# Kernel tuning notes

Measured on AMD Instinct MI355X. Metric: run time of the kernel, lower is better.

## Reference

```python
import jax, jax.numpy as jnp
import numpy as np

M, IN, OUT, R = 8192, 4096, 4096, 16  # tokens, in_features, out_features, lora rank


def setup_inputs() -> dict:
    key = jax.random.key(0)
    k = jax.random.split(key, 7)
    # symmetric int8 quantized activations and weights
    x = jax.random.randint(k[0], (M, IN), -127, 128, dtype=jnp.int8)
    weight = jax.random.randint(k[1], (OUT, IN), -127, 128, dtype=jnp.int8)
    # per-token activation scales and per-output-channel weight scales
    x_scales = jax.random.uniform(k[2], (M,), jnp.float32, 0.5, 1.5) / 127.0
    scales = jax.random.uniform(k[3], (OUT,), jnp.float32, 0.5, 1.5) / 127.0
    bias = jax.random.normal(k[4], (OUT,), jnp.float32)
    # module inits lora_a ~ N(0, 1/r); lora_b is zeros in the module but we use
    # small random values so the LoRA path is numerically exercised
    lora_a = jax.random.normal(k[5], (R, IN), jnp.float32) * (1.0 / R)
    lora_b = jax.random.normal(k[6], (OUT, R), jnp.float32) * 0.02
    return dict(x=x, weight=weight, bias=bias, x_scales=x_scales,
                scales=scales, lora_a=lora_a, lora_b=lora_b, fuse_gelu=1)


def reference(x, weight, bias, x_scales, scales, lora_a, lora_b, fuse_gelu):
    acc = jax.lax.dot_general(x, weight, (((1,), (1,)), ((), ())),
                              preferred_element_type=jnp.int32)
    # dequantize with outer product of per-token and per-channel scales
    main = acc.astype(jnp.float32) * x_scales[:, None] * scales[None, :]
    # LoRA correction on the dequantized activations: (x_deq @ A^T) @ B^T
    x_deq = x.astype(jnp.float32) * x_scales[:, None]          # [M, IN]
    lora = (x_deq @ lora_a.T) @ lora_b.T                        # [M, R] @ [R, OUT]
    out = main + lora + bias[None, :]
    if fuse_gelu:  # static Python flag
        out = jax.nn.gelu(out, approximate=True)  # tanh-approx GELU (CUDA fused path)
    return out
```

## Files before the change

kernel.cpp:

```cpp
#include <hip/hip_runtime.h>

#define M_DIM 8192
#define IN_DIM 4096
#define OUT_DIM 4096

typedef int   v4i __attribute__((ext_vector_type(4)));
typedef short v8s __attribute__((ext_vector_type(8)));
typedef float v4f __attribute__((ext_vector_type(4)));

static __device__ __forceinline__ int pack4(int a, int b, int c, int d) {
    return (a & 255) | ((b & 255) << 8) | ((c & 255) << 16) | ((d & 255) << 24);
}

static __device__ __forceinline__ short f2bf(float f) {
    unsigned u = __float_as_uint(f);
    u = (u + 0x7FFFu + ((u >> 16) & 1u)) >> 16;
    return (short)u;
}

static __device__ __forceinline__ float gelu_tanh(float u) {
    float u2 = u * u;
    float p  = fmaf(u2, 0.0356774081f, 0.7978845608f);
    float v  = u * p;
    float e  = __builtin_amdgcn_exp2f(v * 2.8853900818f);
    float d  = e + 1.0f;
    return u - u * __builtin_amdgcn_rcpf(d);
}

static __device__ __forceinline__ void async_cp16(const signed char* g, signed char* l) {
    __builtin_amdgcn_global_load_lds((const __attribute__((address_space(1))) void*)g,
                                     (__attribute__((address_space(3))) void*)l, 16, 0, 0);
}

__global__ __launch_bounds__(256) void pack_w_kernel(const int* __restrict__ w,
                                                     signed char* __restrict__ w8) {
    size_t i = ((size_t)blockIdx.x * 256 + threadIdx.x) * 16;
    const int4* p = (const int4*)(w + i);
    int4 a = p[0], b = p[1], c = p[2], d = p[3];
    int4 o;
    o.x = pack4(a.x, a.y, a.z, a.w);
    o.y = pack4(b.x, b.y, b.z, b.w);
    o.z = pack4(c.x, c.y, c.z, c.w);
    o.w = pack4(d.x, d.y, d.z, d.w);
    *(int4*)(w8 + i) = o;
}

__global__ __launch_bounds__(256) void pack_x_lora_kernel(const int* __restrict__ x,
                                                          const float* __restrict__ la,
                                                          signed char* __restrict__ x8,
                                                          float* __restrict__ T) {
    __shared__ float red[64 * 257];
    const int t    = threadIdx.x;
    const int row0 = blockIdx.x * 4;
    const int k0   = t * 16;

    float xf[4][16];
#pragma unroll
    for (int g = 0; g < 4; ++g) {
        const int4* xp = (const int4*)(x + (size_t)(row0 + g) * IN_DIM + k0);
        int4 a = xp[0], b = xp[1], c = xp[2], d = xp[3];
        int4 o;
        o.x = pack4(a.x, a.y, a.z, a.w);
        o.y = pack4(b.x, b.y, b.z, b.w);
        o.z = pack4(c.x, c.y, c.z, c.w);
        o.w = pack4(d.x, d.y, d.z, d.w);
        *(int4*)(x8 + (size_t)(row0 + g) * IN_DIM + k0) = o;
        xf[g][0]=(float)a.x;  xf[g][1]=(float)a.y;  xf[g][2]=(float)a.z;  xf[g][3]=(float)a.w;
        xf[g][4]=(float)b.x;  xf[g][5]=(float)b.y;  xf[g][6]=(float)b.z;  xf[g][7]=(float)b.w;
        xf[g][8]=(float)c.x;  xf[g][9]=(float)c.y;  xf[g][10]=(float)c.z; xf[g][11]=(float)c.w;
        xf[g][12]=(float)d.x; xf[g][13]=(float)d.y; xf[g][14]=(float)d.z; xf[g][15]=(float)d.w;
    }

    float acc[4][16];
#pragma unroll
    for (int g = 0; g < 4; ++g)
#pragma unroll
        for (int r = 0; r < 16; ++r) acc[g][r] = 0.0f;

#pragma unroll
    for (int r = 0; r < 16; ++r) {
        const float4* ap = (const float4*)(la + (size_t)r * IN_DIM + k0);
        float4 a0 = ap[0], a1 = ap[1], a2 = ap[2], a3 = ap[3];
        float av[16] = {a0.x,a0.y,a0.z,a0.w, a1.x,a1.y,a1.z,a1.w,
                        a2.x,a2.y,a2.z,a2.w, a3.x,a3.y,a3.z,a3.w};
#pragma unroll
        for (int g = 0; g < 4; ++g) {
#pragma unroll
            for (int j = 0; j < 16; ++j) acc[g][r] = fmaf(xf[g][j], av[j], acc[g][r]);
        }
    }

#pragma unroll
    for (int g = 0; g < 4; ++g)
#pragma unroll
        for (int r = 0; r < 16; ++r) red[(g * 16 + r) * 257 + t] = acc[g][r];
    __syncthreads();

    if (t < 64) {
        float s = 0.0f;
        for (int tt = 0; tt < 256; ++tt) s += red[t * 257 + tt];
        T[(size_t)(row0 + (t >> 4)) * 16 + (t & 15)] = s;
    }
}

__global__ __launch_bounds__(256) void q8_gemm_kernel(
    const signed char* __restrict__ x8, const signed char* __restrict__ w8,
    const float* __restrict__ T, const float* __restrict__ lb,
    const float* __restrict__ bias, const float* __restrict__ xsc,
    const float* __restrict__ wsc, const int* __restrict__ gflag,
    float* __restrict__ out) {
    __shared__ __align__(16) signed char Ald[128 * 64];
    __shared__ __align__(16) signed char Bld[128 * 64];
    __shared__ __align__(16) short Tb[128 * 32];
    __shared__ __align__(16) short Bb[128 * 32];
    __shared__ float xs_t[128], ws_t[128], bias_t[128];

    const int tid  = threadIdx.x;
    const int lane = tid & 63;
    const int wv   = tid >> 6;
    const int wm   = wv >> 1;
    const int wn   = wv & 1;
    const int bn   = blockIdx.x & 31;
    const int bm   = blockIdx.x >> 5;

    const int frow = lane & 15;
    const int fq   = lane >> 4;

    const int srow = wv * 32 + (lane >> 2);
    const int scol = (lane & 3) * 16;
    const signed char* ag0 = x8 + (size_t)(bm * 128 + srow) * IN_DIM + scol;
    const signed char* ag1 = ag0 + 16 * IN_DIM;
    const signed char* bg0 = w8 + (size_t)(bn * 128 + srow) * IN_DIM + scol;
    const signed char* bg1 = bg0 + 16 * IN_DIM;
    signed char* al0 = &Ald[wv * 2048];
    signed char* al1 = al0 + 1024;
    signed char* bl0 = &Bld[wv * 2048];
    signed char* bl1 = bl0 + 1024;

    v4i acc[4][4];
#pragma unroll
    for (int i = 0; i < 4; ++i)
#pragma unroll
        for (int j = 0; j < 4; ++j) acc[i][j] = 0;

    const int abase = (wm * 64 + frow) * 64 + fq * 16;
    const int bbase = (wn * 64 + frow) * 64 + fq * 16;

    for (int kk = 0; kk < IN_DIM / 64; ++kk) {
        __syncthreads();
        const size_t ko = (size_t)kk * 64;
        async_cp16(ag0 + ko, al0);
        async_cp16(ag1 + ko, al1);
        async_cp16(bg0 + ko, bl0);
        async_cp16(bg1 + ko, bl1);
        __syncthreads();

        v4i av[4], bv[4];
#pragma unroll
        for (int mt = 0; mt < 4; ++mt) av[mt] = *(const v4i*)(Ald + abase + mt * 1024);
#pragma unroll
        for (int nt = 0; nt < 4; ++nt) bv[nt] = *(const v4i*)(Bld + bbase + nt * 1024);
#pragma unroll
        for (int mt = 0; mt < 4; ++mt)
#pragma unroll
            for (int nt = 0; nt < 4; ++nt)
                acc[mt][nt] = __builtin_amdgcn_mfma_i32_16x16x64_i8(av[mt], bv[nt],
                                                                    acc[mt][nt], 0, 0, 0);
    }

    {
        const int row = tid >> 1, half = tid & 1;
        const float4* tp = (const float4*)(T + (size_t)(bm * 128 + row) * 16 + half * 8);
        float4 f0 = tp[0], f1 = tp[1];
        short* dst = &Tb[row * 32 + half * 8];
        dst[0] = f2bf(f0.x); dst[1] = f2bf(f0.y); dst[2] = f2bf(f0.z); dst[3] = f2bf(f0.w);
        dst[4] = f2bf(f1.x); dst[5] = f2bf(f1.y); dst[6] = f2bf(f1.z); dst[7] = f2bf(f1.w);
        short* dz = &Tb[row * 32 + 16 + half * 8];
#pragma unroll
        for (int j = 0; j < 8; ++j) dz[j] = 0;

        const float4* bp = (const float4*)(lb + (size_t)(bn * 128 + row) * 16 + half * 8);
        float4 g0 = bp[0], g1 = bp[1];
        short* db = &Bb[row * 32 + half * 8];
        db[0] = f2bf(g0.x); db[1] = f2bf(g0.y); db[2] = f2bf(g0.z); db[3] = f2bf(g0.w);
        db[4] = f2bf(g1.x); db[5] = f2bf(g1.y); db[6] = f2bf(g1.z); db[7] = f2bf(g1.w);
        short* dbz = &Bb[row * 32 + 16 + half * 8];
#pragma unroll
        for (int j = 0; j < 8; ++j) dbz[j] = 0;
    }
    if (tid < 128) {
        xs_t[tid]   = xsc[bm * 128 + tid];
        ws_t[tid]   = wsc[bn * 128 + tid];
        bias_t[tid] = bias[bn * 128 + tid];
    }
    __syncthreads();

    const bool dg = (*gflag) != 0;

    v8s tb[4], bbf[4];
#pragma unroll
    for (int mt = 0; mt < 4; ++mt)
        tb[mt] = *(const v8s*)(&Tb[(wm * 64 + mt * 16 + frow) * 32 + fq * 8]);
#pragma unroll
    for (int nt = 0; nt < 4; ++nt)
        bbf[nt] = *(const v8s*)(&Bb[(wn * 64 + nt * 16 + frow) * 32 + fq * 8]);

#pragma unroll
    for (int mt = 0; mt < 4; ++mt) {
#pragma unroll
        for (int nt = 0; nt < 4; ++nt) {
            const int ncol  = wn * 64 + nt * 16 + frow;
            const float wsv = ws_t[ncol];
            const float bv  = bias_t[ncol];
            v4f fa;
            fa[0] = (float)acc[mt][nt][0] * wsv;
            fa[1] = (float)acc[mt][nt][1] * wsv;
            fa[2] = (float)acc[mt][nt][2] * wsv;
            fa[3] = (float)acc[mt][nt][3] * wsv;
            fa = __builtin_amdgcn_mfma_f32_16x16x32_bf16(tb[mt], bbf[nt], fa, 0, 0, 0);
#pragma unroll
            for (int r = 0; r < 4; ++r) {
                const int ml = wm * 64 + mt * 16 + fq * 4 + r;
                float u = fmaf(xs_t[ml], fa[r], bv);
                if (dg) u = gelu_tanh(u);
                out[(size_t)(bm * 128 + ml) * OUT_DIM + bn * 128 + ncol] = u;
            }
        }
    }
}

extern "C" void kernel_launch(void* const* d_in, const int* in_sizes, int n_in,
                              void* d_out, int out_size, void* d_ws, size_t ws_size,
                              hipStream_t stream) {
    const int*   x     = (const int*)d_in[0];
    const int*   wt    = (const int*)d_in[1];
    const float* bias  = (const float*)d_in[2];
    const float* xsc   = (const float*)d_in[3];
    const float* wsc   = (const float*)d_in[4];
    const float* la    = (const float*)d_in[5];
    const float* lb    = (const float*)d_in[6];
    const int*   gflag = (const int*)d_in[7];
    float* out = (float*)d_out;

    signed char* x8 = (signed char*)d_ws;
    signed char* w8 = x8 + (size_t)M_DIM * IN_DIM;
    float* T = (float*)(w8 + (size_t)OUT_DIM * IN_DIM);

    pack_w_kernel<<<(OUT_DIM * (size_t)IN_DIM) / (16 * 256), 256, 0, stream>>>(wt, w8);
    pack_x_lora_kernel<<<M_DIM / 4, 256, 0, stream>>>(x, la, x8, T);
    q8_gemm_kernel<<<(M_DIM / 128) * (OUT_DIM / 128), 256, 0, stream>>>(
        x8, w8, T, lb, bias, xsc, wsc, gflag, out);
}
```

Measured before the change: 482.7 us.

## Double-buffer GEMM LDS tiles, swizzle layout, and move LoRA projection to MFMA

The int8 GEMM main loop now double-buffers its A/B tiles in a single shared buffer and issues the next k-tile's async loads before computing on the current one. An XOR swizzle on the column offset is meant to cut LDS bank conflicts, and an occupancy hint is added to launch bounds. The LoRA down-projection moves out of a scalar FMA kernel with a large shared reduction into a bf16 MFMA kernel over packed int8 x, with lora_a pre-converted to bf16 in the w8 scratch region before w is packed. The pack kernels are rewritten for coalesced access. Converting x and lora_a to bf16 in the LoRA path changes precision.

```diff
diff --git a/kernel.cpp b/kernel.cpp
--- a/kernel.cpp
+++ b/kernel.cpp
@@ -16,6 +16,11 @@
     unsigned u = __float_as_uint(f);
     u = (u + 0x7FFFu + ((u >> 16) & 1u)) >> 16;
     return (short)u;
+}
+
+static __device__ __forceinline__ short i2bf(int v) {
+    float f = (float)v;
+    return (short)(__float_as_uint(f) >> 16);
 }
 
 static __device__ __forceinline__ float gelu_tanh(float u) {
@@ -23,8 +28,7 @@
     float p  = fmaf(u2, 0.0356774081f, 0.7978845608f);
     float v  = u * p;
     float e  = __builtin_amdgcn_exp2f(v * 2.8853900818f);
-    float d  = e + 1.0f;
-    return u - u * __builtin_amdgcn_rcpf(d);
+    return u - u * __builtin_amdgcn_rcpf(e + 1.0f);
 }
 
 static __device__ __forceinline__ void async_cp16(const signed char* g, signed char* l) {
@@ -32,88 +36,71 @@
                                      (__attribute__((address_space(3))) void*)l, 16, 0, 0);
 }
 
-__global__ __launch_bounds__(256) void pack_w_kernel(const int* __restrict__ w,
-                                                     signed char* __restrict__ w8) {
-    size_t i = ((size_t)blockIdx.x * 256 + threadIdx.x) * 16;
-    const int4* p = (const int4*)(w + i);
-    int4 a = p[0], b = p[1], c = p[2], d = p[3];
-    int4 o;
-    o.x = pack4(a.x, a.y, a.z, a.w);
-    o.y = pack4(b.x, b.y, b.z, b.w);
-    o.z = pack4(c.x, c.y, c.z, c.w);
-    o.w = pack4(d.x, d.y, d.z, d.w);
-    *(int4*)(w8 + i) = o;
-}
-
-__global__ __launch_bounds__(256) void pack_x_lora_kernel(const int* __restrict__ x,
-                                                          const float* __restrict__ la,
-                                                          signed char* __restrict__ x8,
-                                                          float* __restrict__ T) {
-    __shared__ float red[64 * 257];
-    const int t    = threadIdx.x;
-    const int row0 = blockIdx.x * 4;
-    const int k0   = t * 16;
-
-    float xf[4][16];
-#pragma unroll
-    for (int g = 0; g < 4; ++g) {
-        const int4* xp = (const int4*)(x + (size_t)(row0 + g) * IN_DIM + k0);
-        int4 a = xp[0], b = xp[1], c = xp[2], d = xp[3];
-        int4 o;
-        o.x = pack4(a.x, a.y, a.z, a.w);
-        o.y = pack4(b.x, b.y, b.z, b.w);
-        o.z = pack4(c.x, c.y, c.z, c.w);
-        o.w = pack4(d.x, d.y, d.z, d.w);
-        *(int4*)(x8 + (size_t)(row0 + g) * IN_DIM + k0) = o;
-        xf[g][0]=(float)a.x;  xf[g][1]=(float)a.y;  xf[g][2]=(float)a.z;  xf[g][3]=(float)a.w;
-        xf[g][4]=(float)b.x;  xf[g][5]=(float)b.y;  xf[g][6]=(float)b.z;  xf[g][7]=(float)b.w;
-        xf[g][8]=(float)c.x;  xf[g][9]=(float)c.y;  xf[g][10]=(float)c.z; xf[g][11]=(float)c.w;
-        xf[g][12]=(float)d.x; xf[g][13]=(float)d.y; xf[g][14]=(float)d.z; xf[g][15]=(float)d.w;
-    }
-
-    float acc[4][16];
-#pragma unroll
-    for (int g = 0; g < 4; ++g)
-#pragma unroll
-        for (int r = 0; r < 16; ++r) acc[g][r] = 0.0f;
-
-#pragma unroll
-    for (int r = 0; r < 16; ++r) {
-        const float4* ap = (const float4*)(la + (size_t)r * IN_DIM + k0);
-        float4 a0 = ap[0], a1 = ap[1], a2 = ap[2], a3 = ap[3];
-        float av[16] = {a0.x,a0.y,a0.z,a0.w, a1.x,a1.y,a1.z,a1.w,
-                        a2.x,a2.y,a2.z,a2.w, a3.x,a3.y,a3.z,a3.w};
-#pragma unroll
-        for (int g = 0; g < 4; ++g) {
-#pragma unroll
-            for (int j = 0; j < 16; ++j) acc[g][r] = fmaf(xf[g][j], av[j], acc[g][r]);
-        }
-    }
-
-#pragma unroll
-    for (int g = 0; g < 4; ++g)
-#pragma unroll
-        for (int r = 0; r < 16; ++r) red[(g * 16 + r) * 257 + t] = acc[g][r];
+__global__ __launch_bounds__(256) void pack_i32_i8_kernel(const int* __restrict__ src,
+                                                          signed char* __restrict__ dst) {
+    const int t = threadIdx.x;
+    const size_t blk = (size_t)blockIdx.x;
+    const int4* p = (const int4*)src + blk * 1024;
+    int* q = (int*)dst + blk * 1024;
+    int4 v0 = p[t], v1 = p[256 + t], v2 = p[512 + t], v3 = p[768 + t];
+    q[t]       = pack4(v0.x, v0.y, v0.z, v0.w);
+    q[256 + t] = pack4(v1.x, v1.y, v1.z, v1.w);
+    q[512 + t] = pack4(v2.x, v2.y, v2.z, v2.w);
+    q[768 + t] = pack4(v3.x, v3.y, v3.z, v3.w);
+}
+
+__global__ __launch_bounds__(256) void pack_a_kernel(const float* __restrict__ la,
+                                                     short* __restrict__ a16) {
+    size_t i = ((size_t)blockIdx.x * 256 + threadIdx.x) * 8;
+    const float4* p = (const float4*)(la + i);
+    float4 a = p[0], b = p[1];
+    v8s o;
+    o[0] = f2bf(a.x); o[1] = f2bf(a.y); o[2] = f2bf(a.z); o[3] = f2bf(a.w);
+    o[4] = f2bf(b.x); o[5] = f2bf(b.y); o[6] = f2bf(b.z); o[7] = f2bf(b.w);
+    *(v8s*)(a16 + i) = o;
+}
+
+__global__ __launch_bounds__(256) void lora_t_kernel(const signed char* __restrict__ x8,
+                                                     const short* __restrict__ a16,
+                                                     float* __restrict__ T) {
+    __shared__ float red[4 * 256];
+    const int tid = threadIdx.x;
+    const int lane = tid & 63, wv = tid >> 6;
+    const int fr = lane & 15, fq = lane >> 4;
+    const int m0 = blockIdx.x * 16;
+
+    const signed char* bx = x8 + (size_t)(m0 + fr) * IN_DIM + wv * 1024 + fq * 8;
+    const short*       ba = a16 + (size_t)fr * IN_DIM + wv * 1024 + fq * 8;
+
+    v4f acc = {0.f, 0.f, 0.f, 0.f};
+#pragma unroll 4
+    for (int kt = 0; kt < 32; ++kt) {
+        int2 w = *(const int2*)(bx + kt * 32);
+        int lo = w.x, hi = w.y;
+        v8s xa;
+        xa[0] = i2bf((lo << 24) >> 24); xa[1] = i2bf((lo << 16) >> 24);
+        xa[2] = i2bf((lo << 8) >> 24);  xa[3] = i2bf(lo >> 24);
+        xa[4] = i2bf((hi << 24) >> 24); xa[5] = i2bf((hi << 16) >> 24);
+        xa[6] = i2bf((hi << 8) >> 24);  xa[7] = i2bf(hi >> 24);
+        v8s aa = *(const v8s*)(ba + kt * 32);
+        acc = __builtin_amdgcn_mfma_f32_16x16x32_bf16(xa, aa, acc, 0, 0, 0);
+    }
+    *(v4f*)&red[wv * 256 + lane * 4] = acc;
     __syncthreads();
 
-    if (t < 64) {
-        float s = 0.0f;
-        for (int tt = 0; tt < 256; ++tt) s += red[t * 257 + tt];
-        T[(size_t)(row0 + (t >> 4)) * 16 + (t & 15)] = s;
-    }
-}
-
-__global__ __launch_bounds__(256) void q8_gemm_kernel(
+    float s = red[tid] + red[256 + tid] + red[512 + tid] + red[768 + tid];
+    int sl = tid >> 2, j = tid & 3;
+    int row = ((sl >> 4) << 2) + j, col = sl & 15;
+    T[(size_t)(m0 + row) * 16 + col] = s;
+}
+
+__global__ __launch_bounds__(256, 4) void q8_gemm_kernel(
     const signed char* __restrict__ x8, const signed char* __restrict__ w8,
     const float* __restrict__ T, const float* __restrict__ lb,
     const float* __restrict__ bias, const float* __restrict__ xsc,
     const float* __restrict__ wsc, const int* __restrict__ gflag,
     float* __restrict__ out) {
-    __shared__ __align__(16) signed char Ald[128 * 64];
-    __shared__ __align__(16) signed char Bld[128 * 64];
-    __shared__ __align__(16) short Tb[128 * 32];
-    __shared__ __align__(16) short Bb[128 * 32];
-    __shared__ float xs_t[128], ws_t[128], bias_t[128];
+    __shared__ __align__(16) signed char smem[32768];
 
     const int tid  = threadIdx.x;
     const int lane = tid & 63;
@@ -122,20 +109,19 @@
     const int wn   = wv & 1;
     const int bn   = blockIdx.x & 31;
     const int bm   = blockIdx.x >> 5;
-
-    const int frow = lane & 15;
+    const int fr   = lane & 15;
     const int fq   = lane >> 4;
 
     const int srow = wv * 32 + (lane >> 2);
-    const int scol = (lane & 3) * 16;
+    const int scol = (((lane & 3) ^ ((lane >> 2) & 3)) & 3) * 16;
     const signed char* ag0 = x8 + (size_t)(bm * 128 + srow) * IN_DIM + scol;
     const signed char* ag1 = ag0 + 16 * IN_DIM;
     const signed char* bg0 = w8 + (size_t)(bn * 128 + srow) * IN_DIM + scol;
     const signed char* bg1 = bg0 + 16 * IN_DIM;
-    signed char* al0 = &Ald[wv * 2048];
-    signed char* al1 = al0 + 1024;
-    signed char* bl0 = &Bld[wv * 2048];
-    signed char* bl1 = bl0 + 1024;
+    signed char* sA0 = smem + wv * 2048;
+    signed char* sB0 = smem + 8192 + wv * 2048;
+    signed char* sA1 = smem + 16384 + wv * 2048;
+    signed char* sB1 = smem + 24576 + wv * 2048;
 
     v4i acc[4][4];
 #pragma unroll
@@ -143,23 +129,34 @@
 #pragma unroll
         for (int j = 0; j < 4; ++j) acc[i][j] = 0;
 
-    const int abase = (wm * 64 + frow) * 64 + fq * 16;
-    const int bbase = (wn * 64 + frow) * 64 + fq * 16;
-
-    for (int kk = 0; kk < IN_DIM / 64; ++kk) {
+    const int rot    = ((fq ^ fr) & 3) * 16;
+    const int abase0 = (wm * 64 + fr) * 64 + rot;
+    const int bbase0 = (wn * 64 + fr) * 64 + rot;
+
+    async_cp16(ag0, sA0); async_cp16(ag1, sA0 + 1024);
+    async_cp16(bg0, sB0); async_cp16(bg1, sB0 + 1024);
+
+#pragma unroll 2
+    for (int kk = 0; kk < 64; ++kk) {
         __syncthreads();
-        const size_t ko = (size_t)kk * 64;
-        async_cp16(ag0 + ko, al0);
-        async_cp16(ag1 + ko, al1);
-        async_cp16(bg0 + ko, bl0);
-        async_cp16(bg1 + ko, bl1);
-        __syncthreads();
+        if (kk + 1 < 64) {
+            const size_t ko = (size_t)(kk + 1) * 64;
+            if (kk & 1) {
+                async_cp16(ag0 + ko, sA0); async_cp16(ag1 + ko, sA0 + 1024);
+                async_cp16(bg0 + ko, sB0); async_cp16(bg1 + ko, sB0 + 1024);
+            } else {
+                async_cp16(ag0 + ko, sA1); async_cp16(ag1 + ko, sA1 + 1024);
+                async_cp16(bg0 + ko, sB1); async_cp16(bg1 + ko, sB1 + 1024);
+            }
+        }
+        const signed char* Ab = smem + ((kk & 1) ? 16384 : 0);
+        const signed char* Bb = Ab + 8192;
 
         v4i av[4], bv[4];
 #pragma unroll
-        for (int mt = 0; mt < 4; ++mt) av[mt] = *(const v4i*)(Ald + abase + mt * 1024);
-#pragma unroll
-        for (int nt = 0; nt < 4; ++nt) bv[nt] = *(const v4i*)(Bld + bbase + nt * 1024);
+        for (int mt = 0; mt < 4; ++mt) av[mt] = *(const v4i*)(Ab + abase0 + mt * 1024);
+#pragma unroll
+        for (int nt = 0; nt < 4; ++nt) bv[nt] = *(const v4i*)(Bb + bbase0 + nt * 1024);
 #pragma unroll
         for (int mt = 0; mt < 4; ++mt)
 #pragma unroll
@@ -167,6 +164,13 @@
                 acc[mt][nt] = __builtin_amdgcn_mfma_i32_16x16x64_i8(av[mt], bv[nt],
                                                                     acc[mt][nt], 0, 0, 0);
     }
+
+    __syncthreads();
+    short* Tb     = (short*)smem;
+    short* Bbs    = (short*)(smem + 8192);
+    float* xs_t   = (float*)(smem + 16384);
+    float* ws_t   = xs_t + 128;
+    float* bias_t = ws_t + 128;
 
     {
         const int row = tid >> 1, half = tid & 1;
@@ -181,10 +185,10 @@
 
         const float4* bp = (const float4*)(lb + (size_t)(bn * 128 + row) * 16 + half * 8);
         float4 g0 = bp[0], g1 = bp[1];
-        short* db = &Bb[row * 32 + half * 8];
+        short* db = &Bbs[row * 32 + half * 8];
         db[0] = f2bf(g0.x); db[1] = f2bf(g0.y); db[2] = f2bf(g0.z); db[3] = f2bf(g0.w);
         db[4] = f2bf(g1.x); db[5] = f2bf(g1.y); db[6] = f2bf(g1.z); db[7] = f2bf(g1.w);
-        short* dbz = &Bb[row * 32 + 16 + half * 8];
+        short* dbz = &Bbs[row * 32 + 16 + half * 8];
 #pragma unroll
         for (int j = 0; j < 8; ++j) dbz[j] = 0;
     }
@@ -200,16 +204,16 @@
     v8s tb[4], bbf[4];
 #pragma unroll
     for (int mt = 0; mt < 4; ++mt)
-        tb[mt] = *(const v8s*)(&Tb[(wm * 64 + mt * 16 + frow) * 32 + fq * 8]);
+        tb[mt] = *(const v8s*)(&Tb[(wm * 64 + mt * 16 + fr) * 32 + fq * 8]);
 #pragma unroll
     for (int nt = 0; nt < 4; ++nt)
-        bbf[nt] = *(const v8s*)(&Bb[(wn * 64 + nt * 16 + frow) * 32 + fq * 8]);
+        bbf[nt] = *(const v8s*)(&Bbs[(wn * 64 + nt * 16 + fr) * 32 + fq * 8]);
 
 #pragma unroll
     for (int mt = 0; mt < 4; ++mt) {
 #pragma unroll
         for (int nt = 0; nt < 4; ++nt) {
-            const int ncol  = wn * 64 + nt * 16 + frow;
+            const int ncol  = wn * 64 + nt * 16 + fr;
             const float wsv = ws_t[ncol];
             const float bv  = bias_t[ncol];
             v4f fa;
@@ -245,9 +249,12 @@
     signed char* x8 = (signed char*)d_ws;
     signed char* w8 = x8 + (size_t)M_DIM * IN_DIM;
     float* T = (float*)(w8 + (size_t)OUT_DIM * IN_DIM);
-
-    pack_w_kernel<<<(OUT_DIM * (size_t)IN_DIM) / (16 * 256), 256, 0, stream>>>(wt, w8);
-    pack_x_lora_kernel<<<M_DIM / 4, 256, 0, stream>>>(x, la, x8, T);
+    short* a16 = (short*)w8;
+
+    pack_i32_i8_kernel<<<(size_t)M_DIM * IN_DIM / 4096, 256, 0, stream>>>(x, x8);
+    pack_a_kernel<<<16 * IN_DIM / (8 * 256), 256, 0, stream>>>(la, a16);
+    lora_t_kernel<<<M_DIM / 16, 256, 0, stream>>>(x8, a16, T);
+    pack_i32_i8_kernel<<<(size_t)OUT_DIM * IN_DIM / 4096, 256, 0, stream>>>(wt, w8);
     q8_gemm_kernel<<<(M_DIM / 128) * (OUT_DIM / 128), 256, 0, stream>>>(
         x8, w8, T, lb, bias, xsc, wsc, gflag, out);
 }
```

Result: faster. 454.5 us (-5.8%).
